# Performance work log

Hardware: AMD Instinct MI355X
Metric: run time of the kernel (lower is better)

## Reference

```python
import jax, jax.numpy as jnp
import numpy as np

HEADS = 8
DIM_HEAD = 64
RADIUS = 0.2
NSAMPLE = 8
EPS = 1e-5


def setup_inputs() -> dict:
    key = jax.random.key(0)
    ks = jax.random.split(key, 6)
    b, l, n, dim = 2, 4, 1024, 512
    inner = HEADS * DIM_HEAD
    xyzs = jax.random.uniform(ks[0], (b, l, n, 3), jnp.float32)
    feature = jax.random.normal(ks[1], (b, l, n, dim), jnp.float32)
    gamma = jnp.ones((dim,), jnp.float32)
    beta = jnp.zeros((dim,), jnp.float32)
    w_qkv = jax.random.normal(ks[2], (dim, 3 * inner), jnp.float32) * 0.02
    w_spatial = jax.random.normal(ks[3], (3, DIM_HEAD), jnp.float32) * 0.02
    w_out = jax.random.normal(ks[4], (inner, dim), jnp.float32) * 0.02
    b_out = jnp.zeros((dim,), jnp.float32)
    return {"xyzs": xyzs, "feature": feature, "gamma": gamma, "beta": beta,
            "w_qkv": w_qkv, "w_spatial": w_spatial, "w_out": w_out, "b_out": b_out}


def ball_query(ref, query):
    """pointnet2-style ball query. ref:(B,N,3), query:(B,M,3) -> (B,M,NSAMPLE) int32.
    Takes the first (lowest-index) NSAMPLE in-radius points, pads with the first
    found index; all-zeros if no point is in radius (matches CUDA kernel)."""
    d2 = jnp.sum((query[:, :, None, :] - ref[:, None, :, :]) ** 2, axis=-1)  # (B,M,N)
    mask = d2 < RADIUS ** 2
    nref = ref.shape[1]
    score = jnp.where(mask, -jnp.arange(nref, dtype=jnp.float32), -jnp.inf)
    vals, pos = jax.lax.top_k(score, NSAMPLE)  # smallest in-radius indices first
    valid = vals > -jnp.inf
    first = jnp.where(valid[..., :1], pos[..., :1], 0)
    return jnp.where(valid, pos, first)


def _forward(xyzs, feature, gamma, beta, w_qkv, w_spatial, w_out, b_out):
    b, l, n, dim = feature.shape
    h, dh = HEADS, DIM_HEAD
    inner = h * dh
    scale = dh ** -0.5
    # LayerNorm over channel dim
    mu = jnp.mean(feature, -1, keepdims=True)
    var = jnp.var(feature, -1, keepdims=True)
    normf = (feature - mu) * jax.lax.rsqrt(var + EPS) * gamma + beta
    qkv = normf @ w_qkv
    q, k, v = jnp.split(qkv, 3, axis=-1)          # each (b, l, n, inner)
    xyz_flat = xyzs.reshape(b * l, n, 3)
    k_flat = k.reshape(b * l, n, inner)
    v_flat = v.reshape(b * l, n, inner)
    bidx = jnp.arange(b * l)[:, None, None]

    def per_frame(q_i, xyz_i):
        # q_i: (b, n, inner) queries of frame i; xyz_i: (b, n, 3)
        # frame-i points query neighbors inside every frame of the video
        qxyz = jnp.broadcast_to(xyz_i[:, None], (b, l, n, 3)).reshape(b * l, n, 3)
        idx = ball_query(xyz_flat, qxyz)           # (b*l, n, 8)
        g_k = k_flat[bidx, idx]                    # (b*l, n, 8, inner)
        g_v = v_flat[bidx, idx]
        g_xyz = xyz_flat[bidx, idx]                # (b*l, n, 8, 3)
        disp = g_xyz - qxyz[:, :, None]            # (b*l, n, 8, 3)
        # '(b l) n k (h d) -> b n h (l k) d'
        keys = g_k.reshape(b, l, n, NSAMPLE, h, dh).transpose(0, 2, 4, 1, 3, 5).reshape(b, n, h, l * NSAMPLE, dh)
        vals = g_v.reshape(b, l, n, NSAMPLE, h, dh).transpose(0, 2, 4, 1, 3, 5).reshape(b, n, h, l * NSAMPLE, dh)
        qh = q_i.reshape(b, n, h, dh)
        logits = jnp.einsum('bnhd,bnhjd->bnhj', qh, keys) * scale
        attn = jax.nn.softmax(logits, axis=-1)     # (b, n, h, l*8)
        # 'b l n k d -> b n (l k) d'
        dis = disp.reshape(b, l, n, NSAMPLE, 3).transpose(0, 2, 1, 3, 4).reshape(b, n, l * NSAMPLE, 3)
        dis_attn = jnp.max(attn[..., None] * dis[:, :, None], axis=3)  # (b, n, h, 3)
        dis_attn = (dis_attn @ w_spatial).reshape(b, n, inner)         # spatial_op
        attnout = jnp.einsum('bnhj,bnhjd->bnhd', attn, vals).reshape(b, n, inner)
        return attnout + dis_attn

    q_frames = jnp.moveaxis(q, 1, 0)               # (l, b, n, inner)
    xyz_frames = jnp.moveaxis(xyzs, 1, 0)          # (l, b, n, 3)
    frames = jax.vmap(per_frame)(q_frames, xyz_frames)   # (l, b, n, inner)
    frame_result = jnp.moveaxis(frames, 0, 1)      # (b, l, n, inner)
    out = jax.nn.gelu(frame_result @ w_out + b_out, approximate=False)
    return out + feature


def reference(xyzs, feature, gamma, beta, w_qkv, w_spatial, w_out, b_out):
    return _forward(xyzs, feature, gamma, beta, w_qkv, w_spatial, w_out, b_out)
```

## Files before the change

kernel.cpp:

```cpp
#include <hip/hip_runtime.h>
#include <hip/hip_bf16.h>

#define B_ 2
#define L_ 4
#define N_ 1024
#define DIM_ 512
#define INNER_ 512
#define HEADS_ 8
#define DH_ 64
#define NS_ 8
#define NFR_ (B_ * L_)
#define ROWS_ (B_ * L_ * N_)

typedef unsigned short u16;
typedef __attribute__((ext_vector_type(8))) short bf16x8;
typedef __attribute__((ext_vector_type(4))) float f32x4;

__device__ inline float bf2f(u16 u) {
    union { unsigned i; float f; } c; c.i = ((unsigned)u) << 16; return c.f;
}
__device__ inline float bflo(unsigned v) {
    union { unsigned i; float f; } c; c.i = v << 16; return c.f;
}
__device__ inline float bfhi(unsigned v) {
    union { unsigned i; float f; } c; c.i = v & 0xffff0000u; return c.f;
}
__device__ inline u16 f2bf(float x) {
    __hip_bfloat16 h = __float2bfloat16(x);
    return *reinterpret_cast<u16*>(&h);
}

__device__ inline void load_lds16(const void* g, void* l) {
    __builtin_amdgcn_global_load_lds(
        (const __attribute__((address_space(1))) unsigned*)g,
        (__attribute__((address_space(3))) unsigned*)l, 16, 0, 0);
}

#if __has_builtin(__builtin_amdgcn_fdot2_f32_bf16)
typedef __bf16 bf2v __attribute__((ext_vector_type(2)));
__device__ inline float dot8(bf16x8 a, bf16x8 b, float acc) {
    union U { bf16x8 v; bf2v p[4]; };
    U ua, ub; ua.v = a; ub.v = b;
    #pragma unroll
    for (int i = 0; i < 4; ++i)
        acc = __builtin_amdgcn_fdot2_f32_bf16(ua.p[i], ub.p[i], acc, false);
    return acc;
}
#else
__device__ inline float dot8(bf16x8 a, bf16x8 b, float acc) {
    #pragma unroll
    for (int e = 0; e < 8; ++e) acc += bf2f((u16)a[e]) * bf2f((u16)b[e]);
    return acc;
}
#endif

#define RPAD_(r) ((r) + ((r) >> 4))

__global__ __launch_bounds__(256) void prep_kernel(
    const float* __restrict__ wqkv, const float* __restrict__ wout,
    u16* __restrict__ wqkvT, u16* __restrict__ woutT,
    const float* __restrict__ feat, const float* __restrict__ gamma,
    const float* __restrict__ beta, u16* __restrict__ normf,
    const float* __restrict__ xyz, int* __restrict__ idxt)
{
    __shared__ union {
        float tile[64][65];
        struct { float rx[1088], ry[1088], rz[1088]; } bq;
        float red[4];
    } sm;

    int blk = blockIdx.x;
    int t = threadIdx.x;

    if (blk < 256) {
        const float* src; u16* dst; int R, C, tr, tc;
        int b = blk;
        if (b < 192) { src = wqkv; dst = wqkvT; R = 512; C = 1536; tr = b / 24; tc = b % 24; }
        else { b -= 192; src = wout; dst = woutT; R = 512; C = 512; tr = b / 8; tc = b % 8; }
        int r0 = tr * 64, c0 = tc * 64;

        int rr = t >> 2, cs = (t & 3) * 16;
        const float* sp = src + (size_t)(r0 + rr) * C + c0 + cs;
        #pragma unroll
        for (int e = 0; e < 16; e += 4) {
            f32x4 v = *(const f32x4*)(sp + e);
            sm.tile[rr][cs + e + 0] = v[0];
            sm.tile[rr][cs + e + 1] = v[1];
            sm.tile[rr][cs + e + 2] = v[2];
            sm.tile[rr][cs + e + 3] = v[3];
        }
        __syncthreads();

        int c = t >> 2, ks = (t & 3) * 16;
        u16 outv[16];
        #pragma unroll
        for (int e = 0; e < 16; ++e) outv[e] = f2bf(sm.tile[ks + e][c]);
        u16* dp = dst + (size_t)(c0 + c) * R + r0 + ks;
        *(bf16x8*)(dp)     = *(bf16x8*)&outv[0];
        *(bf16x8*)(dp + 8) = *(bf16x8*)&outv[8];

    } else if (blk < 256 + ROWS_) {
        int row = blk - 256;
        const float* fr = feat + (size_t)row * DIM_;
        float x0 = fr[t], x1 = fr[t + 256];

        float s = x0 + x1;
        #pragma unroll
        for (int off = 32; off; off >>= 1) s += __shfl_xor(s, off, 64);
        if ((t & 63) == 0) sm.red[t >> 6] = s;
        __syncthreads();
        float mu = (sm.red[0] + sm.red[1] + sm.red[2] + sm.red[3]) * (1.0f / 512.0f);
        __syncthreads();

        float d0 = x0 - mu, d1 = x1 - mu;
        float q = d0 * d0 + d1 * d1;
        #pragma unroll
        for (int off = 32; off; off >>= 1) q += __shfl_xor(q, off, 64);
        if ((t & 63) == 0) sm.red[t >> 6] = q;
        __syncthreads();
        float var = (sm.red[0] + sm.red[1] + sm.red[2] + sm.red[3]) * (1.0f / 512.0f);
        float inv = rsqrtf(var + 1e-5f);

        normf[(size_t)row * DIM_ + t]       = f2bf(d0 * inv * gamma[t]       + beta[t]);
        normf[(size_t)row * DIM_ + t + 256] = f2bf(d1 * inv * gamma[t + 256] + beta[t + 256]);

    } else {
        #pragma clang fp contract(off)
        int bb = blk - (256 + ROWS_);
        int chunk = bb & 255;
        int combo = bb >> 8;
        int jf = combo & 3;
        int bi = combo >> 2;

        const float* ref = xyz + (size_t)((bi * L_ + jf) * N_) * 3;
        for (int p = t; p < N_; p += 256) {
            sm.bq.rx[RPAD_(p)] = ref[p * 3 + 0];
            sm.bq.ry[RPAD_(p)] = ref[p * 3 + 1];
            sm.bq.rz[RPAD_(p)] = ref[p * 3 + 2];
        }
        __syncthreads();

        int wave = t >> 6;
        int lane = t & 63;
        int n = chunk * 4 + wave;
        int base = lane * 17;
        int r0 = lane * 16;

        for (int qi = 0; qi < L_; ++qi) {
            const float* qp = xyz + (size_t)((bi * L_ + qi) * N_ + n) * 3;
            float qx = qp[0], qy = qp[1], qz = qp[2];

            unsigned mask = 0;
            #pragma unroll
            for (int j = 0; j < 16; ++j) {
                float dx = qx - sm.bq.rx[base + j];
                float dy = qy - sm.bq.ry[base + j];
                float dz = qz - sm.bq.rz[base + j];
                float d2 = dx * dx + dy * dy;
                d2 = d2 + dz * dz;
                if (d2 < 0.04f) mask |= (1u << j);
            }

            int cnt = __popc(mask);
            int x = cnt;
            #pragma unroll
            for (int off = 1; off < 64; off <<= 1) {
                int y = __shfl_up(x, off, 64);
                if (lane >= off) x += y;
            }
            int pre = x - cnt;
            int total = __shfl(x, 63, 64);

            int localFirst = mask ? (r0 + __builtin_ctz(mask)) : 0x7fffffff;
            int gfirst = localFirst;
            #pragma unroll
            for (int off = 32; off; off >>= 1) gfirst = min(gfirst, __shfl_xor(gfirst, off, 64));

            int* o = idxt + ((size_t)((qi * B_ + bi) * N_ + n)) * 32 + jf * NS_;

            unsigned m = mask;
            int pos = pre;
            while (m && pos < NS_) {
                int j = __builtin_ctz(m);
                o[pos] = r0 + j;
                m &= m - 1;
                ++pos;
            }
            if (lane == 0) {
                int padv = (total > 0) ? gfirst : 0;
                for (int s = (total < NS_ ? total : NS_); s < NS_; ++s) o[s] = padv;
            }
        }
    }
}

__global__ __launch_bounds__(512) void gemm_bt(
    const u16* __restrict__ A, const u16* __restrict__ Bt,
    u16* __restrict__ Cb16, float* __restrict__ Cf32,
    int M, int N, int K, int nb128, int mode,
    const float* __restrict__ bias, const float* __restrict__ resid)
{
    __shared__ u16 As[2][128 * 32];
    __shared__ u16 Bs[2][128 * 32];

    int bx = blockIdx.x % nb128;
    int by = blockIdx.x / nb128;
    int m0 = by * 128, n0 = bx * 128;
    int t = threadIdx.x;
    int wave = t >> 6, lane = t & 63;
    int lr = lane & 15, quad = lane >> 4;
    int wm = (wave >> 2) * 64;
    int wn = (wave & 3) * 32;

    int rs = t >> 2;
    int kcs = (t & 3) * 8;

    f32x4 acc[4][2];
    #pragma unroll
    for (int i = 0; i < 4; ++i)
        #pragma unroll
        for (int j = 0; j < 2; ++j)
            acc[i][j] = {0.f, 0.f, 0.f, 0.f};

    int NT = K >> 5;

    load_lds16(A  + (size_t)(m0 + rs) * K + kcs, &As[0][t * 8]);
    load_lds16(Bt + (size_t)(n0 + rs) * K + kcs, &Bs[0][t * 8]);
    __syncthreads();

    int cur = 0;
    for (int kt = 0; kt < NT; ++kt) {
        if (kt + 1 < NT) {
            int k0 = (kt + 1) << 5;
            load_lds16(A  + (size_t)(m0 + rs) * K + k0 + kcs, &As[cur ^ 1][t * 8]);
            load_lds16(Bt + (size_t)(n0 + rs) * K + k0 + kcs, &Bs[cur ^ 1][t * 8]);
        }

        bf16x8 af[4], bfr[2];
        #pragma unroll
        for (int mb = 0; mb < 4; ++mb)
            af[mb] = *(const bf16x8*)&As[cur][(wm + mb * 16 + lr) * 32 + quad * 8];
        #pragma unroll
        for (int nb = 0; nb < 2; ++nb)
            bfr[nb] = *(const bf16x8*)&Bs[cur][(wn + nb * 16 + lr) * 32 + quad * 8];
        #pragma unroll
        for (int mb = 0; mb < 4; ++mb)
            #pragma unroll
            for (int nb = 0; nb < 2; ++nb)
                acc[mb][nb] = __builtin_amdgcn_mfma_f32_16x16x32_bf16(
                    af[mb], bfr[nb], acc[mb][nb], 0, 0, 0);

        __syncthreads();
        cur ^= 1;
    }

    #pragma unroll
    for (int mb = 0; mb < 4; ++mb) {
        #pragma unroll
        for (int nb = 0; nb < 2; ++nb) {
            int col = n0 + wn + nb * 16 + lr;
            #pragma unroll
            for (int r = 0; r < 4; ++r) {
                int row = m0 + wm + mb * 16 + quad * 4 + r;
                float x = acc[mb][nb][r];
                if (mode == 1) {
                    x += bias[col];
                    float gl = 0.5f * x * (1.0f + erff(x * 0.70710678118654752f));
                    Cf32[(size_t)row * N + col] = gl + resid[(size_t)row * N + col];
                } else {
                    Cb16[(size_t)row * N + col] = f2bf(x);
                }
            }
        }
    }
}

__global__ __launch_bounds__(256, 4) void attn_kernel(
    const float* __restrict__ xyz, const u16* __restrict__ qkv,
    const int* __restrict__ idxt, const float* __restrict__ wsp,
    u16* __restrict__ fres)
{
    int x = blockIdx.x & 7;
    int bi = x >> 2;
    int qi = x & 3;
    int n = blockIdx.x >> 3;

    int t = threadIdx.x;
    int wave = t >> 6, lane = t & 63;

    int qrow = (bi * L_ + qi) * N_ + n;
    int qq = (qi * B_ + bi) * N_ + n;

    __shared__ int grow_s[32];
    __shared__ float nx_s[32], ny_s[32], nz_s[32];
    __shared__ float lg_s[HEADS_][33];
    __shared__ float a_s[HEADS_][32];
    __shared__ float da_s[HEADS_][3];

    bf16x8 qf = *(const bf16x8*)(qkv + (size_t)qrow * 1536 + lane * 8);

    if (t < 32) {
        int idx = idxt[(size_t)qq * 32 + t];
        int jf = t >> 3;
        int kr = (bi * L_ + jf) * N_ + idx;
        grow_s[t] = kr;
        nx_s[t] = xyz[(size_t)kr * 3 + 0];
        ny_s[t] = xyz[(size_t)kr * 3 + 1];
        nz_s[t] = xyz[(size_t)kr * 3 + 2];
    }
    __syncthreads();

    bf16x8 kf[8];
    #pragma unroll
    for (int r = 0; r < 8; ++r) {
        int kr = __builtin_amdgcn_readfirstlane(grow_s[wave * 8 + r]);
        const char* kbase = (const char*)qkv + (size_t)kr * 3072 + 1024;
        kf[r] = *(const bf16x8*)(kbase + lane * 16);
    }
    __builtin_amdgcn_sched_barrier(0);

    #pragma unroll
    for (int r = 0; r < 8; ++r) {
        float p = dot8(kf[r], qf, 0.f);
        p += __shfl_xor(p, 1, 64);
        p += __shfl_xor(p, 2, 64);
        p += __shfl_xor(p, 4, 64);
        if ((lane & 7) == 0) lg_s[lane >> 3][wave * 8 + r] = p * 0.125f;
    }
    __syncthreads();

    int hh = lane >> 5;
    int j = lane & 31;
    int h = wave * 2 + hh;

    float lg = lg_s[h][j];
    float mx = lg;
    #pragma unroll
    for (int off = 16; off; off >>= 1) mx = fmaxf(mx, __shfl_xor(mx, off, 64));
    float e = expf(lg - mx);
    float sum = e;
    #pragma unroll
    for (int off = 16; off; off >>= 1) sum += __shfl_xor(sum, off, 64);
    float a = e / sum;
    a_s[h][j] = a;

    float qx = xyz[(size_t)qrow * 3 + 0];
    float qy = xyz[(size_t)qrow * 3 + 1];
    float qz = xyz[(size_t)qrow * 3 + 2];
    float tx = a * (nx_s[j] - qx);
    float ty = a * (ny_s[j] - qy);
    float tz = a * (nz_s[j] - qz);
    #pragma unroll
    for (int off = 16; off; off >>= 1) {
        tx = fmaxf(tx, __shfl_xor(tx, off, 64));
        ty = fmaxf(ty, __shfl_xor(ty, off, 64));
        tz = fmaxf(tz, __shfl_xor(tz, off, 64));
    }
    if (j == 0) { da_s[h][0] = tx; da_s[h][1] = ty; da_s[h][2] = tz; }

    __syncthreads();

    int dd = j * 2;
    unsigned vbyte = (1024u + (unsigned)h * 64u + (unsigned)dd) * 2u;
    unsigned vv[32];
    #pragma unroll
    for (int s = 0; s < 32; ++s) {
        int r = __builtin_amdgcn_readfirstlane(grow_s[s]);
        const char* vbase = (const char*)qkv + (size_t)r * 3072;
        vv[s] = *(const unsigned*)(vbase + vbyte);
    }
    __builtin_amdgcn_sched_barrier(0);

    float o0 = 0.f, o1 = 0.f;
    #pragma unroll
    for (int s = 0; s < 32; ++s) {
        float at = a_s[h][s];
        o0 += at * bflo(vv[s]);
        o1 += at * bfhi(vv[s]);
    }
    float dax = da_s[h][0], day = da_s[h][1], daz = da_s[h][2];
    float sp0 = dax * wsp[dd]     + day * wsp[64 + dd]     + daz * wsp[128 + dd];
    float sp1 = dax * wsp[dd + 1] + day * wsp[64 + dd + 1] + daz * wsp[128 + dd + 1];

    u16* op = fres + (size_t)qrow * INNER_ + h * 64 + dd;
    unsigned outw = (unsigned)f2bf(o0 + sp0) | ((unsigned)f2bf(o1 + sp1) << 16);
    *(unsigned*)op = outw;
}

extern "C" void kernel_launch(void* const* d_in, const int* in_sizes, int n_in,
                              void* d_out, int out_size, void* d_ws, size_t ws_size,
                              hipStream_t stream) {
    const float* xyz   = (const float*)d_in[0];
    const float* feat  = (const float*)d_in[1];
    const float* gamma = (const float*)d_in[2];
    const float* beta  = (const float*)d_in[3];
    const float* wqkv  = (const float*)d_in[4];
    const float* wsp   = (const float*)d_in[5];
    const float* wout  = (const float*)d_in[6];
    const float* bout  = (const float*)d_in[7];
    float* out = (float*)d_out;

    char* ws = (char*)d_ws;
    u16* normf = (u16*)ws;                 ws += (size_t)ROWS_ * DIM_ * 2;
    u16* wqkvT = (u16*)ws;                 ws += (size_t)3 * INNER_ * DIM_ * 2;
    u16* woutT = (u16*)ws;                 ws += (size_t)DIM_ * INNER_ * 2;
    u16* qkv   = (u16*)ws;                 ws += (size_t)ROWS_ * 3 * INNER_ * 2;
    int* idxt  = (int*)ws;                 ws += (size_t)L_ * NFR_ * N_ * NS_ * 4;
    u16* fres  = normf;

    prep_kernel<<<256 + ROWS_ + 2048, 256, 0, stream>>>(
        wqkv, wout, wqkvT, woutT, feat, gamma, beta, normf, xyz, idxt);
    gemm_bt<<<64 * 12, 512, 0, stream>>>(normf, wqkvT, qkv, nullptr,
                                         ROWS_, 3 * INNER_, DIM_, 12, 0, nullptr, nullptr);
    attn_kernel<<<ROWS_, 256, 0, stream>>>(xyz, qkv, idxt, wsp, fres);
    gemm_bt<<<64 * 4, 512, 0, stream>>>(fres, woutT, nullptr, out,
                                        ROWS_, DIM_, INNER_, 4, 1, bout, feat);
}
```

Baseline: 182.0 us.

## Store K and V in FP8 to halve gather traffic in attention

The QKV GEMM epilogue now writes K and V columns as FP8 (e4m3) bytes into a separate buffer, while Q stays bf16. The attention kernel gathers these 1-byte values and decodes them with the hardware packed-convert builtins, or a software fallback, before the dot products and the weighted sum. The aim is to halve the bytes moved by the random neighbour gathers of K and V. In exchange, K and V lose precision relative to the fp32 reference, which may break tolerance, and the scattered byte stores in the GEMM epilogue may write less efficiently.

```diff
diff --git a/kernel.cpp b/kernel.cpp
--- a/kernel.cpp
+++ b/kernel.cpp
@@ -13,21 +13,70 @@
 #define ROWS_ (B_ * L_ * N_)
 
 typedef unsigned short u16;
+typedef unsigned char u8;
 typedef __attribute__((ext_vector_type(8))) short bf16x8;
 typedef __attribute__((ext_vector_type(4))) float f32x4;
+typedef __attribute__((ext_vector_type(2))) float f32x2;
 
 __device__ inline float bf2f(u16 u) {
     union { unsigned i; float f; } c; c.i = ((unsigned)u) << 16; return c.f;
-}
-__device__ inline float bflo(unsigned v) {
-    union { unsigned i; float f; } c; c.i = v << 16; return c.f;
-}
-__device__ inline float bfhi(unsigned v) {
-    union { unsigned i; float f; } c; c.i = v & 0xffff0000u; return c.f;
 }
 __device__ inline u16 f2bf(float x) {
     __hip_bfloat16 h = __float2bfloat16(x);
     return *reinterpret_cast<u16*>(&h);
+}
+
+#if __has_builtin(__builtin_amdgcn_cvt_pk_f32_fp8) && __has_builtin(__builtin_amdgcn_cvt_pk_fp8_f32)
+#define F8_HW 1
+#endif
+
+__device__ inline float f8_dec1(unsigned b) {
+    unsigned e = (b >> 3) & 15, m = b & 7;
+    float v;
+    if (e == 0) v = (float)m * 0.001953125f;
+    else { union { unsigned i; float f; } c; c.i = ((e + 120u) << 23) | (m << 20); v = c.f; }
+    return (b & 0x80) ? -v : v;
+}
+__device__ inline unsigned f8_enc1(float x) {
+    union { float f; unsigned u; } c; c.f = x;
+    unsigned s = (c.u >> 31) << 7;
+    float a = fabsf(x);
+    if (a >= 448.f) return s | 0x7e;
+    if (a < 0.015625f) {
+        int m = (int)(a * 512.f + 0.5f); if (m > 7) m = 7;
+        return s | (unsigned)m;
+    }
+    int E; float fr = frexpf(a, &E);
+    int m4 = (int)(fr * 16.f + 0.5f);
+    int e = E - 1 + 7;
+    if (m4 == 16) { m4 = 8; e += 1; }
+    if (e >= 16) return s | 0x7e;
+    return s | (unsigned)(e << 3) | (unsigned)(m4 - 8);
+}
+__device__ inline u8 f8_enc(float x) {
+#ifdef F8_HW
+    return (u8)(__builtin_amdgcn_cvt_pk_fp8_f32(x, 0.f, 0, false) & 0xff);
+#else
+    return (u8)f8_enc1(x);
+#endif
+}
+__device__ inline void f8_dec2(unsigned w, float& lo, float& hi) {
+#ifdef F8_HW
+    f32x2 r = __builtin_amdgcn_cvt_pk_f32_fp8((int)w, false);
+    lo = r[0]; hi = r[1];
+#else
+    lo = f8_dec1(w & 0xffu); hi = f8_dec1((w >> 8) & 0xffu);
+#endif
+}
+__device__ inline void f8_dec4(unsigned w, float* o) {
+#ifdef F8_HW
+    f32x2 a = __builtin_amdgcn_cvt_pk_f32_fp8((int)w, false);
+    f32x2 b = __builtin_amdgcn_cvt_pk_f32_fp8((int)w, true);
+    o[0] = a[0]; o[1] = a[1]; o[2] = b[0]; o[3] = b[1];
+#else
+    o[0] = f8_dec1(w & 0xffu); o[1] = f8_dec1((w >> 8) & 0xffu);
+    o[2] = f8_dec1((w >> 16) & 0xffu); o[3] = f8_dec1(w >> 24);
+#endif
 }
 
 __device__ inline void load_lds16(const void* g, void* l) {
@@ -35,24 +84,6 @@
         (const __attribute__((address_space(1))) unsigned*)g,
         (__attribute__((address_space(3))) unsigned*)l, 16, 0, 0);
 }
-
-#if __has_builtin(__builtin_amdgcn_fdot2_f32_bf16)
-typedef __bf16 bf2v __attribute__((ext_vector_type(2)));
-__device__ inline float dot8(bf16x8 a, bf16x8 b, float acc) {
-    union U { bf16x8 v; bf2v p[4]; };
-    U ua, ub; ua.v = a; ub.v = b;
-    #pragma unroll
-    for (int i = 0; i < 4; ++i)
-        acc = __builtin_amdgcn_fdot2_f32_bf16(ua.p[i], ub.p[i], acc, false);
-    return acc;
-}
-#else
-__device__ inline float dot8(bf16x8 a, bf16x8 b, float acc) {
-    #pragma unroll
-    for (int e = 0; e < 8; ++e) acc += bf2f((u16)a[e]) * bf2f((u16)b[e]);
-    return acc;
-}
-#endif
 
 #define RPAD_(r) ((r) + ((r) >> 4))
 
@@ -198,7 +229,8 @@
     const u16* __restrict__ A, const u16* __restrict__ Bt,
     u16* __restrict__ Cb16, float* __restrict__ Cf32,
     int M, int N, int K, int nb128, int mode,
-    const float* __restrict__ bias, const float* __restrict__ resid)
+    const float* __restrict__ bias, const float* __restrict__ resid,
+    u8* __restrict__ kv8)
 {
     __shared__ u16 As[2][128 * 32];
     __shared__ u16 Bs[2][128 * 32];
@@ -267,8 +299,10 @@
                     x += bias[col];
                     float gl = 0.5f * x * (1.0f + erff(x * 0.70710678118654752f));
                     Cf32[(size_t)row * N + col] = gl + resid[(size_t)row * N + col];
+                } else if (!kv8 || col < 512) {
+                    Cb16[(size_t)row * N + col] = f2bf(x);
                 } else {
-                    Cb16[(size_t)row * N + col] = f2bf(x);
+                    kv8[(size_t)row * 1024 + (col - 512)] = f8_enc(x);
                 }
             }
         }
@@ -277,8 +311,8 @@
 
 __global__ __launch_bounds__(256, 4) void attn_kernel(
     const float* __restrict__ xyz, const u16* __restrict__ qkv,
-    const int* __restrict__ idxt, const float* __restrict__ wsp,
-    u16* __restrict__ fres)
+    const u8* __restrict__ kv8, const int* __restrict__ idxt,
+    const float* __restrict__ wsp, u16* __restrict__ fres)
 {
     int x = blockIdx.x & 7;
     int bi = x >> 2;
@@ -298,6 +332,9 @@
     __shared__ float da_s[HEADS_][3];
 
     bf16x8 qf = *(const bf16x8*)(qkv + (size_t)qrow * 1536 + lane * 8);
+    float qv[8];
+    #pragma unroll
+    for (int e = 0; e < 8; ++e) qv[e] = bf2f((u16)qf[e]);
 
     if (t < 32) {
         int idx = idxt[(size_t)qq * 32 + t];
@@ -310,18 +347,22 @@
     }
     __syncthreads();
 
-    bf16x8 kf[8];
+    uint2 k8[8];
     #pragma unroll
     for (int r = 0; r < 8; ++r) {
         int kr = __builtin_amdgcn_readfirstlane(grow_s[wave * 8 + r]);
-        const char* kbase = (const char*)qkv + (size_t)kr * 3072 + 1024;
-        kf[r] = *(const bf16x8*)(kbase + lane * 16);
+        k8[r] = *(const uint2*)(kv8 + (size_t)kr * 1024 + lane * 8);
     }
     __builtin_amdgcn_sched_barrier(0);
 
     #pragma unroll
     for (int r = 0; r < 8; ++r) {
-        float p = dot8(kf[r], qf, 0.f);
+        float kd[8];
+        f8_dec4(k8[r].x, &kd[0]);
+        f8_dec4(k8[r].y, &kd[4]);
+        float p = 0.f;
+        #pragma unroll
+        for (int e = 0; e < 8; ++e) p += kd[e] * qv[e];
         p += __shfl_xor(p, 1, 64);
         p += __shfl_xor(p, 2, 64);
         p += __shfl_xor(p, 4, 64);
@@ -361,13 +402,12 @@
     __syncthreads();
 
     int dd = j * 2;
-    unsigned vbyte = (1024u + (unsigned)h * 64u + (unsigned)dd) * 2u;
-    unsigned vv[32];
+    unsigned vboff = 512u + (unsigned)h * 64u + (unsigned)dd;
+    unsigned short vv[32];
     #pragma unroll
     for (int s = 0; s < 32; ++s) {
         int r = __builtin_amdgcn_readfirstlane(grow_s[s]);
-        const char* vbase = (const char*)qkv + (size_t)r * 3072;
-        vv[s] = *(const unsigned*)(vbase + vbyte);
+        vv[s] = *(const unsigned short*)(kv8 + (size_t)r * 1024 + vboff);
     }
     __builtin_amdgcn_sched_barrier(0);
 
@@ -375,8 +415,10 @@
     #pragma unroll
     for (int s = 0; s < 32; ++s) {
         float at = a_s[h][s];
-        o0 += at * bflo(vv[s]);
-        o1 += at * bfhi(vv[s]);
+        float vlo, vhi;
+        f8_dec2((unsigned)vv[s], vlo, vhi);
+        o0 += at * vlo;
+        o1 += at * vhi;
     }
     float dax = da_s[h][0], day = da_s[h][1], daz = da_s[h][2];
     float sp0 = dax * wsp[dd]     + day * wsp[64 + dd]     + daz * wsp[128 + dd];
@@ -406,13 +448,14 @@
     u16* woutT = (u16*)ws;                 ws += (size_t)DIM_ * INNER_ * 2;
     u16* qkv   = (u16*)ws;                 ws += (size_t)ROWS_ * 3 * INNER_ * 2;
     int* idxt  = (int*)ws;                 ws += (size_t)L_ * NFR_ * N_ * NS_ * 4;
+    u8*  kv8   = (u8*)ws;                  ws += (size_t)ROWS_ * 1024;
     u16* fres  = normf;
 
     prep_kernel<<<256 + ROWS_ + 2048, 256, 0, stream>>>(
         wqkv, wout, wqkvT, woutT, feat, gamma, beta, normf, xyz, idxt);
     gemm_bt<<<64 * 12, 512, 0, stream>>>(normf, wqkvT, qkv, nullptr,
-                                         ROWS_, 3 * INNER_, DIM_, 12, 0, nullptr, nullptr);
-    attn_kernel<<<ROWS_, 256, 0, stream>>>(xyz, qkv, idxt, wsp, fres);
+                                         ROWS_, 3 * INNER_, DIM_, 12, 0, nullptr, nullptr, kv8);
+    attn_kernel<<<ROWS_, 256, 0, stream>>>(xyz, qkv, kv8, idxt, wsp, fres);
     gemm_bt<<<64 * 4, 512, 0, stream>>>(fres, woutT, nullptr, out,
-                                        ROWS_, DIM_, INNER_, 4, 1, bout, feat);
-}
+                                        ROWS_, DIM_, INNER_, 4, 1, bout, feat, nullptr);
+}
```

New measurement: 182.6 us. Within noise of the previous version (+0.3%).
